# Kernel optimization log

Measured on AMD Instinct MI355X. Metric: run time of the kernel, lower is better.

The kernel has to match this reference:

```python
import jax, jax.numpy as jnp
import numpy as np

NUM_EMBEDDINGS = 8192
EMBEDDING_DIM = 256
COMMITMENT_COST = 0.25
TAU = 0.9
B, C, H, W = 4, NUM_EMBEDDINGS, 32, 32


def setup_inputs() -> dict:
    key = jax.random.key(0)
    k1, k2, k3 = jax.random.split(key, 3)
    x = jax.random.normal(k1, (B, C, H, W), dtype=jnp.float32)
    # nn.Embedding weight initialized uniform(-0.5, 0.5)
    emb_weight = jax.random.uniform(k2, (NUM_EMBEDDINGS, EMBEDDING_DIM),
                                    dtype=jnp.float32, minval=-0.5, maxval=0.5)
    # standard Gumbel(0,1) noise, sampled once for reproducibility
    u = jax.random.uniform(k3, (B, C, H, W), dtype=jnp.float32,
                           minval=1e-10, maxval=1.0)
    gumbel_noise = -jnp.log(-jnp.log(u))
    return {"x": x, "emb_weight": emb_weight, "gumbel_noise": gumbel_noise}


def reference(x, emb_weight, gumbel_noise):
    n = x.shape[1]  # num_embeddings (channel dim)
    # --- gumbel_softmax(tau=0.9, hard=True, dim=1) ---
    y_soft = jax.nn.softmax((x + gumbel_noise) / TAU, axis=1)  # [B,N,H,W]
    idx = jnp.argmax(y_soft, axis=1)                           # [B,H,W]
    y_hard = jax.nn.one_hot(idx, n, axis=1, dtype=y_soft.dtype)
    # straight-through estimator
    one_hot = y_soft + jax.lax.stop_gradient(y_hard - y_soft)  # [B,N,H,W]
    # --- codebook lookup as one-hot matmul ---
    quantized = jnp.einsum('bnhw,nd->bdhw', one_hot, emb_weight)
    # --- KL(uniform || q) with F.kl_div semantics, reduction='batchmean' ---
    # logits rearranged to b (h w) n and log_softmax over n == log_softmax over axis=1 of x
    log_qy = jax.nn.log_softmax(x, axis=1)                     # [B,N,H,W]
    t = 1.0 / n
    # pointwise kl = target * (log(target) - log_qy); batchmean divides by B
    kl_div = jnp.sum(t * (jnp.log(jnp.asarray(t, x.dtype)) - log_qy)) / x.shape[0]
    return quantized, COMMITMENT_COST * kl_div, one_hot
```

## Files before the change

### kernel.cpp

```cpp
#include <hip/hip_runtime.h>
#include <math.h>

#define BSZ 4
#define CCH 8192
#define HW  1024
#define DEMB 256
#define NPOS (BSZ*HW)
#define QSIZE (BSZ*DEMB*HW)
#define KLOFF QSIZE
#define OHOFF (QSIZE+1)
#define OHSZ  ((size_t)BSZ*CCH*HW)

template<int CPB>
__global__ __launch_bounds__(256) void vq_phase1(const float* __restrict__ x,
                                                 const float* __restrict__ g,
                                                 float* __restrict__ out,
                                                 float* __restrict__ ws) {
    constexpr int NCH = CCH / CPB;
    constexpr int P   = NPOS * NCH;
    int bid = blockIdx.x;
    int q = bid % NCH;
    int b = bid / NCH;
    int t = threadIdx.x;
    int c0 = q * CPB;
    size_t row0 = (size_t)(b * CCH + c0);
    size_t base = row0 * HW + 4 * t;

    float best[4]; int bidx[4]; float s[4], sx[4];
#pragma unroll
    for (int j = 0; j < 4; j++) { best[j] = -INFINITY; bidx[j] = 0; s[j] = 0.f; sx[j] = 0.f; }

    const float4 z4 = make_float4(0.f, 0.f, 0.f, 0.f);
#pragma unroll 4
    for (int c = 0; c < CPB; c++) {
        size_t a = base + (size_t)c * HW;
        float4 xv = *(const float4*)(x + a);
        float4 gv = *(const float4*)(g + a);
        *(float4*)(out + QSIZE + a) = z4;
        int cc = c0 + c;
        float xa[4] = {xv.x, xv.y, xv.z, xv.w};
        float ga[4] = {gv.x, gv.y, gv.z, gv.w};
#pragma unroll
        for (int j = 0; j < 4; j++) {
            float z = xa[j] + ga[j];
            if (z > best[j]) { best[j] = z; bidx[j] = cc; }
            s[j]  += __expf(xa[j]);
            sx[j] += xa[j];
        }
    }

    if (b == BSZ - 1 && q == NCH - 1 && t == 255)
        out[QSIZE + OHSZ] = 0.f;

    int o = q * NPOS + b * HW + 4 * t;
    float* wbest = ws;
    int*   widx  = (int*)(ws + P);
    float* wsum  = ws + 2 * (size_t)P;
    float* wsx   = ws + 3 * (size_t)P;
    *(float4*)(wbest + o) = make_float4(best[0], best[1], best[2], best[3]);
    *(int4*)  (widx  + o) = make_int4(bidx[0], bidx[1], bidx[2], bidx[3]);
    *(float4*)(wsum  + o) = make_float4(s[0], s[1], s[2], s[3]);
    *(float4*)(wsx   + o) = make_float4(sx[0], sx[1], sx[2], sx[3]);
}

template<int CPB>
__global__ __launch_bounds__(256) void vq_phase2(float* __restrict__ out,
                                                 float* __restrict__ ws) {
    constexpr int NCH = CCH / CPB;
    constexpr int P   = NPOS * NCH;
    int pos = blockIdx.x * 256 + threadIdx.x;
    const float* wbest = ws;
    const int*   widx  = (const int*)(ws + P);
    const float* wsum  = ws + 2 * (size_t)P;
    const float* wsx   = ws + 3 * (size_t)P;
    int*         fidx  = (int*)(ws + 4 * (size_t)P);

    float fb = -INFINITY; int fi = 0;
    float fs = 0.f, fsx = 0.f;
    for (int q = 0; q < NCH; q++) {
        int o = q * NPOS + pos;
        float v = wbest[o]; int ci = widx[o];
        if (v > fb || (v == fb && ci < fi)) { fb = v; fi = ci; }
        fs  += wsum[o];
        fsx += wsx[o];
    }
    fidx[pos] = fi;

    int b = pos >> 10;
    int hw = pos & (HW - 1);
    out[OHOFF + ((size_t)(b * CCH + fi)) * HW + hw] = 1.0f;

    float lse = __logf(fs);
    const float logt = -9.0109131783f;
    float term = logt + lse - fsx * (1.0f / (float)CCH);

    for (int off = 32; off > 0; off >>= 1) term += __shfl_down(term, off, 64);
    __shared__ float wsuml[4];
    int lane = threadIdx.x & 63, wv = threadIdx.x >> 6;
    if (lane == 0) wsuml[wv] = term;
    __syncthreads();
    if (threadIdx.x == 0) {
        float tt = wsuml[0] + wsuml[1] + wsuml[2] + wsuml[3];
        atomicAdd(out + KLOFF, (0.25f / (float)BSZ) * tt);
    }
}

__global__ __launch_bounds__(256) void vq_phase3(const float* __restrict__ emb,
                                                 const int* __restrict__ fidx,
                                                 float* __restrict__ outq) {
    int u = blockIdx.x * 256 + threadIdx.x;
    int b = u >> 16;
    int r = u & 65535;
    int d = r >> 8;
    int h4 = (r & 255) * 4;
    int pos = (b << 10) + h4;
    float4 v;
    v.x = emb[fidx[pos + 0] * DEMB + d];
    v.y = emb[fidx[pos + 1] * DEMB + d];
    v.z = emb[fidx[pos + 2] * DEMB + d];
    v.w = emb[fidx[pos + 3] * DEMB + d];
    *(float4*)(outq + ((size_t)(b * DEMB + d) << 10) + h4) = v;
}

template<int CPB>
static void launch_all(const float* x, const float* emb, const float* g,
                       float* out, float* ws, hipStream_t stream) {
    constexpr int NCH = CCH / CPB;
    constexpr int P   = NPOS * NCH;
    vq_phase1<CPB><<<dim3(BSZ * NCH), dim3(256), 0, stream>>>(x, g, out, ws);
    vq_phase2<CPB><<<dim3(NPOS / 256), dim3(256), 0, stream>>>(out, ws);
    vq_phase3<<<dim3(QSIZE / 4 / 256), dim3(256), 0, stream>>>(
        emb, (const int*)(ws + 4 * (size_t)P), out);
}

extern "C" void kernel_launch(void* const* d_in, const int* in_sizes, int n_in,
                              void* d_out, int out_size, void* d_ws, size_t ws_size,
                              hipStream_t stream) {
    (void)in_sizes; (void)n_in; (void)out_size;
    const float* x   = (const float*)d_in[0];
    const float* emb = (const float*)d_in[1];
    const float* g   = (const float*)d_in[2];
    float* out = (float*)d_out;
    float* ws  = (float*)d_ws;

    if (ws_size >= (size_t)16 * (NPOS * (CCH / 64)) + 4 * NPOS) {
        launch_all<64>(x, emb, g, out, ws, stream);
    } else if (ws_size >= (size_t)16 * (NPOS * (CCH / 128)) + 4 * NPOS) {
        launch_all<128>(x, emb, g, out, ws, stream);
    } else {
        launch_all<256>(x, emb, g, out, ws, stream);
    }
}
```

Measured before the change: 390.9 us.

## Parallelize phase-2 reduction across chunk groups and shrink phase-1 chunk size

Phase 2 now assigns 16 positions per block, with 16 thread groups each reducing a slice of the chunk partials, then combines them through shared memory. Previously one thread walked every chunk serially and only 16 blocks were launched. The grid grows to 256 blocks, which should hide latency better. The default phase-1 chunk size drops from 64 to 32 channels when the workspace allows, giving more phase-1 blocks at the cost of doubling the partial-result traffic. Phase-2 reads are now only 16-wide coalesced segments.

```diff
diff --git a/kernel.cpp b/kernel.cpp
--- a/kernel.cpp
+++ b/kernel.cpp
@@ -23,8 +23,7 @@
     int b = bid / NCH;
     int t = threadIdx.x;
     int c0 = q * CPB;
-    size_t row0 = (size_t)(b * CCH + c0);
-    size_t base = row0 * HW + 4 * t;
+    size_t base = ((size_t)(b * CCH + c0)) * HW + 4 * t;
 
     float best[4]; int bidx[4]; float s[4], sx[4];
 #pragma unroll
@@ -54,7 +53,7 @@
 
     int o = q * NPOS + b * HW + 4 * t;
     float* wbest = ws;
-    int*   widx  = (int*)(ws + P);
+    int*   widx  = (int*)(ws + (size_t)P);
     float* wsum  = ws + 2 * (size_t)P;
     float* wsx   = ws + 3 * (size_t)P;
     *(float4*)(wbest + o) = make_float4(best[0], best[1], best[2], best[3]);
@@ -68,39 +67,64 @@
                                                  float* __restrict__ ws) {
     constexpr int NCH = CCH / CPB;
     constexpr int P   = NPOS * NCH;
-    int pos = blockIdx.x * 256 + threadIdx.x;
+    constexpr int QPT = NCH / 16;
     const float* wbest = ws;
-    const int*   widx  = (const int*)(ws + P);
+    const int*   widx  = (const int*)(ws + (size_t)P);
     const float* wsum  = ws + 2 * (size_t)P;
     const float* wsx   = ws + 3 * (size_t)P;
     int*         fidx  = (int*)(ws + 4 * (size_t)P);
 
+    int tid = threadIdx.x;
+    int pl = tid & 15;
+    int qg = tid >> 4;
+    int pos0 = blockIdx.x * 16;
+    int pos = pos0 + pl;
+
     float fb = -INFINITY; int fi = 0;
     float fs = 0.f, fsx = 0.f;
-    for (int q = 0; q < NCH; q++) {
+    for (int i = 0; i < QPT; i++) {
+        int q = qg * QPT + i;
         int o = q * NPOS + pos;
         float v = wbest[o]; int ci = widx[o];
         if (v > fb || (v == fb && ci < fi)) { fb = v; fi = ci; }
         fs  += wsum[o];
         fsx += wsx[o];
     }
-    fidx[pos] = fi;
 
-    int b = pos >> 10;
-    int hw = pos & (HW - 1);
-    out[OHOFF + ((size_t)(b * CCH + fi)) * HW + hw] = 1.0f;
+    __shared__ float l_b [16][17];
+    __shared__ int   l_i [16][17];
+    __shared__ float l_s [16][17];
+    __shared__ float l_sx[16][17];
+    __shared__ float tsum[16];
+    l_b [qg][pl] = fb;
+    l_i [qg][pl] = fi;
+    l_s [qg][pl] = fs;
+    l_sx[qg][pl] = fsx;
+    __syncthreads();
 
-    float lse = __logf(fs);
-    const float logt = -9.0109131783f;
-    float term = logt + lse - fsx * (1.0f / (float)CCH);
+    if (tid < 16) {
+        int p = tid;
+        float mb = l_b[0][p]; int mi = l_i[0][p];
+        float ms = l_s[0][p], msx = l_sx[0][p];
+        for (int qq = 1; qq < 16; qq++) {
+            float v = l_b[qq][p]; int ci = l_i[qq][p];
+            if (v > mb || (v == mb && ci < mi)) { mb = v; mi = ci; }
+            ms  += l_s[qq][p];
+            msx += l_sx[qq][p];
+        }
+        int mypos = pos0 + p;
+        fidx[mypos] = mi;
+        int b = mypos >> 10;
+        int hw = mypos & (HW - 1);
+        out[OHOFF + ((size_t)(b * CCH + mi)) * HW + hw] = 1.0f;
 
-    for (int off = 32; off > 0; off >>= 1) term += __shfl_down(term, off, 64);
-    __shared__ float wsuml[4];
-    int lane = threadIdx.x & 63, wv = threadIdx.x >> 6;
-    if (lane == 0) wsuml[wv] = term;
+        const float logt = -9.0109131783f;
+        tsum[p] = logt + __logf(ms) - msx * (1.0f / (float)CCH);
+    }
     __syncthreads();
-    if (threadIdx.x == 0) {
-        float tt = wsuml[0] + wsuml[1] + wsuml[2] + wsuml[3];
+    if (tid == 0) {
+        float tt = 0.f;
+        for (int p = 0; p < 16; p++) tt += tsum[p];
         atomicAdd(out + KLOFF, (0.25f / (float)BSZ) * tt);
     }
 }
@@ -128,7 +152,7 @@
     constexpr int NCH = CCH / CPB;
     constexpr int P   = NPOS * NCH;
     vq_phase1<CPB><<<dim3(BSZ * NCH), dim3(256), 0, stream>>>(x, g, out, ws);
-    vq_phase2<CPB><<<dim3(NPOS / 256), dim3(256), 0, stream>>>(out, ws);
+    vq_phase2<CPB><<<dim3(NPOS / 16), dim3(256), 0, stream>>>(out, ws);
     vq_phase3<<<dim3(QSIZE / 4 / 256), dim3(256), 0, stream>>>(
         emb, (const int*)(ws + 4 * (size_t)P), out);
 }
@@ -143,11 +167,9 @@
     float* out = (float*)d_out;
     float* ws  = (float*)d_ws;
 
-    if (ws_size >= (size_t)16 * (NPOS * (CCH / 64)) + 4 * NPOS) {
+    if (ws_size >= (size_t)16 * ((size_t)NPOS * (CCH / 32)) + 4 * NPOS) {
+        launch_all<32>(x, emb, g, out, ws, stream);
+    } else {
         launch_all<64>(x, emb, g, out, ws, stream);
-    } else if (ws_size >= (size_t)16 * (NPOS * (CCH / 128)) + 4 * NPOS) {
-        launch_all<128>(x, emb, g, out, ws, stream);
-    } else {
-        launch_all<256>(x, emb, g, out, ws, stream);
     }
 }
```

Measured after the change: 349.7 us. 10.5% less time.
